# Performance work log

Hardware: AMD Instinct MI355X
Metric: run time of the kernel (lower is better)

Reference implementation:

```python
import jax, jax.numpy as jnp
from jax import lax
import numpy as np

B, T, H, K = 32, 512, 2048, 128


def setup_inputs() -> dict:
    key = jax.random.key(0)
    k1, k2, k3, k4, k5, k6, k7 = jax.random.split(key, 7)
    hiddens = jax.random.normal(k1, (B, T, H), dtype=jnp.float32)
    mask = jnp.ones((B, T), dtype=jnp.int32)  # mask[:,0] must be on (torchcrf)
    labels = jax.random.randint(k2, (B, T), 0, K)
    W = jax.random.normal(k3, (H, K), dtype=jnp.float32) * 0.02
    b = jnp.zeros((K,), dtype=jnp.float32)
    # torchcrf inits transitions uniform(-0.1, 0.1)
    start_transitions = jax.random.uniform(k4, (K,), minval=-0.1, maxval=0.1)
    end_transitions = jax.random.uniform(k5, (K,), minval=-0.1, maxval=0.1)
    transitions = jax.random.uniform(k6, (K, K), minval=-0.1, maxval=0.1)
    return {"hiddens": hiddens, "mask": mask, "labels": labels, "W": W, "b": b,
            "start_transitions": start_transitions, "end_transitions": end_transitions,
            "transitions": transitions}


def _crf_log_likelihood(emissions, tags, mask, start_t, end_t, trans):
    # emissions: [B,T,K], tags/mask: [B,T]
    Bn, Tn, Kn = emissions.shape
    maskf = mask.astype(emissions.dtype)
    # ---- numerator: score of the gold path ----
    score = start_t[tags[:, 0]] + emissions[jnp.arange(Bn), 0, tags[:, 0]]
    prev, cur = tags[:, :-1], tags[:, 1:]
    emit_cur = jnp.take_along_axis(emissions[:, 1:], cur[..., None], axis=-1)[..., 0]
    score = score + jnp.sum((trans[prev, cur] + emit_cur) * maskf[:, 1:], axis=1)
    last_idx = mask.sum(axis=1).astype(jnp.int32) - 1
    last_tags = jnp.take_along_axis(tags, last_idx[:, None], axis=1)[:, 0]
    score = score + end_t[last_tags]
    # ---- denominator: log partition via stable logsumexp scan ----
    def step(alpha, inp):
        emit_t, m_t = inp  # [B,K], [B]
        nxt = jax.nn.logsumexp(alpha[:, :, None] + trans[None] + emit_t[:, None, :], axis=1)
        alpha = jnp.where(m_t[:, None] > 0, nxt, alpha)
        return alpha, None
    alpha0 = start_t[None, :] + emissions[:, 0]
    emits = jnp.swapaxes(emissions[:, 1:], 0, 1)  # [T-1,B,K]
    ms = jnp.swapaxes(mask[:, 1:], 0, 1)          # [T-1,B]
    alpha, _ = lax.scan(step, alpha0, (emits, ms))
    logZ = jax.nn.logsumexp(alpha + end_t[None, :], axis=1)
    return score - logZ


def _viterbi_decode(emissions, mask, start_t, end_t, trans):
    Bn, Tn, Kn = emissions.shape
    tag_ids = jnp.arange(Kn, dtype=jnp.int32)
    def step(score, inp):
        emit_t, m_t = inp
        cand = score[:, :, None] + trans[None]          # [B,K,K] prev->cur
        bp = jnp.argmax(cand, axis=1).astype(jnp.int32)  # [B,K]
        best = jnp.max(cand, axis=1) + emit_t
        on = m_t[:, None] > 0
        new_score = jnp.where(on, best, score)
        bp = jnp.where(on, bp, tag_ids[None, :])  # identity for padded steps
        return new_score, bp
    score0 = start_t[None, :] + emissions[:, 0]
    emits = jnp.swapaxes(emissions[:, 1:], 0, 1)
    ms = jnp.swapaxes(mask[:, 1:], 0, 1)
    score, history = lax.scan(step, score0, (emits, ms))  # history: [T-1,B,K]
    last_tag = jnp.argmax(score + end_t[None, :], axis=1).astype(jnp.int32)  # [B]
    def back(tag, bp_t):
        tag = jnp.take_along_axis(bp_t, tag[:, None], axis=1)[:, 0]
        return tag, tag
    _, tags_prev = lax.scan(back, last_tag, history, reverse=True)  # [T-1,B]
    tags = jnp.concatenate([tags_prev, last_tag[None, :]], axis=0)  # [T,B]
    return jnp.swapaxes(tags, 0, 1)  # [B,T]


def reference(hiddens, mask, labels, W, b, start_transitions, end_transitions, transitions):
    logits = jnp.einsum('bth,hk->btk', hiddens, W) + b  # emission projection
    decode = _viterbi_decode(logits, mask, start_transitions, end_transitions, transitions)
    llh = _crf_log_likelihood(logits, labels, mask, start_transitions, end_transitions, transitions)
    loss = -jnp.mean(llh)  # -1 * crf(..., reduction='mean')
    return (decode, loss)
```

## Files before the change

kernel.cpp:

```cpp
#include <hip/hip_runtime.h>
#include <hip/hip_bf16.h>
#include <math.h>

#define BB 32
#define TT 512
#define HH 2048
#define KK 128
#define CH 8

__device__ __forceinline__ float quad_add(float x) {
    int a = __builtin_amdgcn_update_dpp(0, __float_as_int(x), 0xB1, 0xF, 0xF, true);
    x += __int_as_float(a);
    int b = __builtin_amdgcn_update_dpp(0, __float_as_int(x), 0x4E, 0xF, 0xF, true);
    x += __int_as_float(b);
    return x;
}
__device__ __forceinline__ float quad_max(float x) {
    int a = __builtin_amdgcn_update_dpp(0, __float_as_int(x), 0xB1, 0xF, 0xF, true);
    x = fmaxf(x, __int_as_float(a));
    int b = __builtin_amdgcn_update_dpp(0, __float_as_int(x), 0x4E, 0xF, 0xF, true);
    x = fmaxf(x, __int_as_float(b));
    return x;
}

__global__ __launch_bounds__(512) void gemm_k(const float* __restrict__ hid,
                                              const float* __restrict__ Wm,
                                              const float* __restrict__ bias,
                                              float* __restrict__ logits,
                                              float* __restrict__ loss_slot) {
    __shared__ union {
        struct { float As[4][16][72]; float Bs[4][16][132]; } s;
        float4 red[16][128];
    } sm;
    const int tid = threadIdx.x, bid = blockIdx.x;
    if (bid == 0 && tid == 0) loss_slot[0] = 0.0f;
    const int g = tid >> 7, lt = tid & 127;
    const int rowBase = bid * 64;
    const int rowg = lt >> 4, colg = lt & 15;
    const int arow = lt >> 1, ahq = lt & 1;

    float acc[8][8];
#pragma unroll
    for (int i = 0; i < 8; i++)
#pragma unroll
        for (int j = 0; j < 8; j++) acc[i][j] = 0.0f;

    const float* hA = hid + (size_t)(rowBase + arow) * HH + g * 512 + ahq * 8;

    float4 a0, a1, bv[4];
    {
        const int h0 = g * 512;
        a0 = *(const float4*)(hA);
        a1 = *(const float4*)(hA + 4);
#pragma unroll
        for (int r = 0; r < 4; ++r) {
            int idx = r * 128 + lt;
            bv[r] = *(const float4*)(Wm + (size_t)(h0 + (idx >> 5)) * KK + (idx & 31) * 4);
        }
    }

    for (int it = 0; it < 32; ++it) {
        __syncthreads();
        const int hb = ahq * 8;
        sm.s.As[g][hb + 0][arow] = a0.x;
        sm.s.As[g][hb + 1][arow] = a0.y;
        sm.s.As[g][hb + 2][arow] = a0.z;
        sm.s.As[g][hb + 3][arow] = a0.w;
        sm.s.As[g][hb + 4][arow] = a1.x;
        sm.s.As[g][hb + 5][arow] = a1.y;
        sm.s.As[g][hb + 6][arow] = a1.z;
        sm.s.As[g][hb + 7][arow] = a1.w;
#pragma unroll
        for (int r = 0; r < 4; ++r) {
            int idx = r * 128 + lt;
            *(float4*)&sm.s.Bs[g][idx >> 5][(idx & 31) * 4] = bv[r];
        }
        __syncthreads();
        if (it + 1 < 32) {
            const int h0 = g * 512 + (it + 1) * 16;
            a0 = *(const float4*)(hA + (it + 1) * 16);
            a1 = *(const float4*)(hA + (it + 1) * 16 + 4);
#pragma unroll
            for (int r = 0; r < 4; ++r) {
                int idx = r * 128 + lt;
                bv[r] = *(const float4*)(Wm + (size_t)(h0 + (idx >> 5)) * KK + (idx & 31) * 4);
            }
        }
#pragma unroll
        for (int h = 0; h < 16; ++h) {
            float4 aL = *(const float4*)&sm.s.As[g][h][rowg * 8];
            float4 aH = *(const float4*)&sm.s.As[g][h][rowg * 8 + 4];
            float4 b0 = *(const float4*)&sm.s.Bs[g][h][colg * 4];
            float4 b1 = *(const float4*)&sm.s.Bs[g][h][64 + colg * 4];
            float ar[8] = {aL.x, aL.y, aL.z, aL.w, aH.x, aH.y, aH.z, aH.w};
            float br[8] = {b0.x, b0.y, b0.z, b0.w, b1.x, b1.y, b1.z, b1.w};
#pragma unroll
            for (int i = 0; i < 8; i++)
#pragma unroll
                for (int j = 0; j < 8; j++) acc[i][j] = fmaf(ar[i], br[j], acc[i][j]);
        }
    }
    __syncthreads();
    for (int gp = 1; gp <= 3; ++gp) {
        if (g == gp) {
#pragma unroll
            for (int i = 0; i < 8; ++i) {
                sm.red[i * 2][lt] = make_float4(acc[i][0], acc[i][1], acc[i][2], acc[i][3]);
                sm.red[i * 2 + 1][lt] = make_float4(acc[i][4], acc[i][5], acc[i][6], acc[i][7]);
            }
        }
        __syncthreads();
        if (g == 0) {
#pragma unroll
            for (int i = 0; i < 8; ++i) {
                float4 r0 = sm.red[i * 2][lt];
                float4 r1 = sm.red[i * 2 + 1][lt];
                acc[i][0] += r0.x; acc[i][1] += r0.y; acc[i][2] += r0.z; acc[i][3] += r0.w;
                acc[i][4] += r1.x; acc[i][5] += r1.y; acc[i][6] += r1.z; acc[i][7] += r1.w;
            }
        }
        __syncthreads();
    }
    if (g == 0) {
        float4 bb0 = *(const float4*)(bias + colg * 4);
        float4 bb1 = *(const float4*)(bias + 64 + colg * 4);
#pragma unroll
        for (int i = 0; i < 8; ++i) {
            int row = rowBase + rowg * 8 + i;
            *(float4*)(logits + (size_t)row * KK + colg * 4) =
                make_float4(acc[i][0] + bb0.x, acc[i][1] + bb0.y, acc[i][2] + bb0.z, acc[i][3] + bb0.w);
            *(float4*)(logits + (size_t)row * KK + 64 + colg * 4) =
                make_float4(acc[i][4] + bb1.x, acc[i][5] + bb1.y, acc[i][6] + bb1.z, acc[i][7] + bb1.w);
        }
    }
}

struct SMemB {
    float ubuf[2][144];
    float red[4];
    float vbuf[128];
};

__global__ __launch_bounds__(256, 1) void scan_k(const float* __restrict__ logits,
                                                 const int* __restrict__ mask,
                                                 const int* __restrict__ labels,
                                                 const float* __restrict__ startT,
                                                 const float* __restrict__ endT,
                                                 const float* __restrict__ trans,
                                                 float* __restrict__ shist,
                                                 float* __restrict__ out) {
    __shared__ SMemB sm;
    const int tid = threadIdx.x;
    const int bid = blockIdx.x;
    const float L2E = 1.4426950408889634f;
    const int s = tid & 3;
    const int jb = tid >> 2;
    const int j0 = jb * 2;
    const int padw = j0 + 4 * (j0 >> 5);
    const int lane = tid & 63;
    const int NCHUNK = TT / CH;

    if (bid < BB) {
        const int b = bid;
        const float* lrow = logits + (size_t)b * TT * KK;
        unsigned long long mb[8];
#pragma unroll
        for (int c = 0; c < 8; ++c) mb[c] = __ballot(mask[b * TT + c * 64 + lane] != 0);
        float V0[32], V1[32];
#pragma unroll
        for (int k = 0; k < 32; k++) {
            V0[k] = exp2f(trans[(s * 32 + k) * KK + j0] * L2E);
            V1[k] = exp2f(trans[(s * 32 + k) * KK + j0 + 1] * L2E);
        }
        float a0_ = (startT[j0] + lrow[j0]) * L2E;
        float a1_ = (startT[j0 + 1] + lrow[j0 + 1]) * L2E;
        float OFF = (startT[0] + lrow[0]) * L2E;
        float S0_ = exp2f(a0_ - OFF);
        float S1_ = exp2f(a1_ - OFF);
        if (s == 0) {
            sm.ubuf[0][padw] = S0_;
            sm.ubuf[0][padw + 1] = S1_;
        }
        float2 emc[CH], emn[CH];
#pragma unroll
        for (int d = 0; d < CH; ++d) emc[d] = *(const float2*)(lrow + (size_t)d * KK + j0);
        __syncthreads();
        int cur = 0;
        for (int c = 0; c < NCHUNK; ++c) {
#pragma unroll
            for (int r = 0; r < CH; ++r) {
                const int t = c * CH + r;
                if (r == 0 && c + 1 < NCHUNK) {
#pragma unroll
                    for (int d = 0; d < CH; ++d)
                        emn[d] = *(const float2*)(lrow + (size_t)((c + 1) * CH + d) * KK + j0);
                }
                if (t > 0 && ((mb[t >> 6] >> (t & 63)) & 1ull)) {
                    const float* ub = &sm.ubuf[cur][s * 36];
                    float u00 = sm.ubuf[cur][0];
                    float uu[32];
#pragma unroll
                    for (int cc = 0; cc < 8; ++cc) {
                        float4 v = *(const float4*)(ub + cc * 4);
                        uu[cc * 4] = v.x; uu[cc * 4 + 1] = v.y; uu[cc * 4 + 2] = v.z; uu[cc * 4 + 3] = v.w;
                    }
                    float2 em = emc[r];
                    float p0e = 0.f, p0o = 0.f, p1e = 0.f, p1o = 0.f;
#pragma unroll
                    for (int k = 0; k < 32; k += 2) {
                        p0e = fmaf(uu[k], V0[k], p0e);
                        p1e = fmaf(uu[k], V1[k], p1e);
                        p0o = fmaf(uu[k + 1], V0[k + 1], p0o);
                        p1o = fmaf(uu[k + 1], V1[k + 1], p1o);
                    }
                    float w0 = quad_add(p0e + p0o);
                    float w1 = quad_add(p1e + p1o);
                    float rinv = __builtin_amdgcn_rcpf(u00);
                    OFF += log2f(u00);
                    S0_ = w0 * (exp2f(em.x * L2E) * rinv);
                    S1_ = w1 * (exp2f(em.y * L2E) * rinv);
                    if (s == 0) {
                        sm.ubuf[cur ^ 1][padw] = S0_;
                        sm.ubuf[cur ^ 1][padw + 1] = S1_;
                    }
                    cur ^= 1;
                }
                __syncthreads();
            }
#pragma unroll
            for (int d = 0; d < CH; ++d) emc[d] = emn[d];
        }
        if (s == 0) {
            sm.vbuf[j0] = log2f(S0_) + endT[j0] * L2E;
            sm.vbuf[j0 + 1] = log2f(S1_) + endT[j0 + 1] * L2E;
        }
        __syncthreads();

        float part = 0.0f;
        for (int tt = tid; tt < TT; tt += 256) {
            if (tt == 0) {
                int l0 = labels[b * TT];
                part += startT[l0] + lrow[l0];
            } else if (mask[b * TT + tt]) {
                int lc = labels[b * TT + tt];
                int lp = labels[b * TT + tt - 1];
                part += trans[lp * KK + lc] + lrow[(size_t)tt * KK + lc];
            }
        }
#pragma unroll
        for (int d = 1; d < 64; d <<= 1) part += __shfl_xor(part, d, 64);
        int wid = tid >> 6;
        if (lane == 0) sm.red[wid] = part;
        __syncthreads();
        if (tid < 64) {
            float v0 = sm.vbuf[tid], v1 = sm.vbuf[tid + 64];
            float mx = fmaxf(v0, v1);
#pragma unroll
            for (int d = 1; d < 64; d <<= 1) mx = fmaxf(mx, __shfl_xor(mx, d, 64));
            float p = exp2f(v0 - mx) + exp2f(v1 - mx);
#pragma unroll
            for (int d = 1; d < 64; d <<= 1) p += __shfl_xor(p, d, 64);
            if (tid == 0) {
                int total = 0;
#pragma unroll
                for (int c = 0; c < 8; ++c) total += __popcll(mb[c]);
                float score = sm.red[0] + sm.red[1] + sm.red[2] + sm.red[3];
                score += endT[labels[b * TT + total - 1]];
                float logZ = (OFF + mx + log2f(p)) * 0.6931471805599453f;
                float llh = score - logZ;
                atomicAdd(out + BB * TT, -llh * (1.0f / 32.0f));
            }
        }
    } else {
        const int b = bid - BB;
        const float* lrow = logits + (size_t)b * TT * KK;
        float* hist = shist + (size_t)b * TT * KK;
        unsigned long long mb[8];
#pragma unroll
        for (int c = 0; c < 8; ++c) mb[c] = __ballot(mask[b * TT + c * 64 + lane] != 0);
        float T0[32], T1[32];
#pragma unroll
        for (int k = 0; k < 32; k++) {
            T0[k] = trans[(s * 32 + k) * KK + j0];
            T1[k] = trans[(s * 32 + k) * KK + j0 + 1];
        }
        float s0_ = startT[j0] + lrow[j0];
        float s1_ = startT[j0 + 1] + lrow[j0 + 1];
        if (s == 0) {
            sm.ubuf[0][padw] = s0_;
            sm.ubuf[0][padw + 1] = s1_;
        } else if (s == 1) {
            *(float2*)(hist + j0) = make_float2(s0_, s1_);
        }
        float2 emc[CH], emn[CH], hb[CH];
#pragma unroll
        for (int d = 0; d < CH; ++d) emc[d] = *(const float2*)(lrow + (size_t)d * KK + j0);
        __syncthreads();
        int cur = 0;
        for (int c = 0; c < NCHUNK; ++c) {
#pragma unroll
            for (int r = 0; r < CH; ++r) {
                const int t = c * CH + r;
                if (r == 0 && c + 1 < NCHUNK) {
#pragma unroll
                    for (int d = 0; d < CH; ++d)
                        emn[d] = *(const float2*)(lrow + (size_t)((c + 1) * CH + d) * KK + j0);
                }
                if (t > 0 && ((mb[t >> 6] >> (t & 63)) & 1ull)) {
                    const float* ub = &sm.ubuf[cur][s * 36];
                    float uu[32];
#pragma unroll
                    for (int cc = 0; cc < 8; ++cc) {
                        float4 v = *(const float4*)(ub + cc * 4);
                        uu[cc * 4] = v.x; uu[cc * 4 + 1] = v.y; uu[cc * 4 + 2] = v.z; uu[cc * 4 + 3] = v.w;
                    }
                    float2 em = emc[r];
                    float m0a = -3.0e38f, m0b = -3.0e38f, m1a = -3.0e38f, m1b = -3.0e38f;
#pragma unroll
                    for (int k = 0; k < 32; k += 4) {
                        m0a = fmaxf(m0a, fmaxf(uu[k] + T0[k], uu[k + 1] + T0[k + 1]));
                        m0b = fmaxf(m0b, fmaxf(uu[k + 2] + T0[k + 2], uu[k + 3] + T0[k + 3]));
                        m1a = fmaxf(m1a, fmaxf(uu[k] + T1[k], uu[k + 1] + T1[k + 1]));
                        m1b = fmaxf(m1b, fmaxf(uu[k + 2] + T1[k + 2], uu[k + 3] + T1[k + 3]));
                    }
                    float m0 = quad_max(fmaxf(m0a, m0b));
                    float m1 = quad_max(fmaxf(m1a, m1b));
                    s0_ = m0 + em.x;
                    s1_ = m1 + em.y;
                    if (s == 0) {
                        sm.ubuf[cur ^ 1][padw] = s0_;
                        sm.ubuf[cur ^ 1][padw + 1] = s1_;
                    }
                    cur ^= 1;
                }
                hb[r] = make_float2(s0_, s1_);
                __syncthreads();
            }
            if (s == 1) {
#pragma unroll
                for (int r = 0; r < CH; ++r)
                    *(float2*)(hist + (size_t)(c * CH + r) * KK + j0) = hb[r];
            }
#pragma unroll
            for (int d = 0; d < CH; ++d) emc[d] = emn[d];
        }
    }
}

__global__ __launch_bounds__(256) void bp_k(const float* __restrict__ shist,
                                            const float* __restrict__ trans,
                                            const int* __restrict__ mask,
                                            unsigned char* __restrict__ bp) {
    const int t = blockIdx.x + 1;
    const int tid = threadIdx.x;
    const int j = tid & 127, bg = tid >> 7;
    __shared__ float sc[BB][KK];
#pragma unroll
    for (int r = 0; r < 4; ++r) {
        int f = tid + r * 256;
        int bb2 = f >> 5, c4 = (f & 31) * 4;
        *(float4*)&sc[bb2][c4] = *(const float4*)&shist[(size_t)bb2 * TT * KK + (size_t)(t - 1) * KK + c4];
    }
    __syncthreads();
    float m[16];
    int idx[16];
#pragma unroll
    for (int c = 0; c < 16; c++) { m[c] = -3.0e38f; idx[c] = 0; }
    for (int i4 = 0; i4 < 32; ++i4) {
        const int ib = i4 * 4;
        float tr0 = trans[(ib + 0) * KK + j];
        float tr1 = trans[(ib + 1) * KK + j];
        float tr2 = trans[(ib + 2) * KK + j];
        float tr3 = trans[(ib + 3) * KK + j];
#pragma unroll
        for (int c = 0; c < 16; c++) {
            float4 s4 = *(const float4*)&sc[bg + 2 * c][ib];
            float c0 = s4.x + tr0, c1 = s4.y + tr1, c2 = s4.z + tr2, c3 = s4.w + tr3;
            if (c0 > m[c]) { m[c] = c0; idx[c] = ib; }
            if (c1 > m[c]) { m[c] = c1; idx[c] = ib + 1; }
            if (c2 > m[c]) { m[c] = c2; idx[c] = ib + 2; }
            if (c3 > m[c]) { m[c] = c3; idx[c] = ib + 3; }
        }
    }
#pragma unroll
    for (int c = 0; c < 16; c++) {
        int bb2 = bg + 2 * c;
        int v = idx[c];
        if (mask[bb2 * TT + t] == 0) v = j;
        bp[(size_t)bb2 * TT * KK + (size_t)t * KK + j] = (unsigned char)v;
    }
}

__global__ __launch_bounds__(512) void bt_k(const float* __restrict__ shist,
                                            const float* __restrict__ endT,
                                            const unsigned char* __restrict__ bp,
                                            float* __restrict__ out) {
    const int b = blockIdx.x;
    const int tid = threadIdx.x;
    const int lane = tid & 63, w = tid >> 6;
    __shared__ float cb[128];
    __shared__ int tagbuf[512];
    __shared__ int handoff;
    if (tid < 128) cb[tid] = shist[(size_t)b * TT * KK + (size_t)(TT - 1) * KK + tid] + endT[tid];
    __syncthreads();
    if (tid == 0) {
        float mm = cb[0];
        int bi = 0;
        for (int i = 1; i < 128; i++)
            if (cb[i] > mm) { mm = cb[i]; bi = i; }
        tagbuf[TT - 1] = bi;
        handoff = bi;
    }
    unsigned int reg[64];
    const unsigned char* bpb = bp + (size_t)b * TT * KK;
#pragma unroll
    for (int r = 0; r < 64; r++) {
        int t_row = w * 64 + 1 + r;
        unsigned int v = 0;
        if (t_row < TT) v = *(const unsigned short*)(bpb + (size_t)t_row * KK + lane * 2);
        reg[r] = v;
    }
    __syncthreads();
    for (int ph = 7; ph >= 0; --ph) {
        if (w == ph) {
            int tag = handoff;
#pragma unroll
            for (int r = 63; r >= 0; --r) {
                int t_row = ph * 64 + 1 + r;
                if (t_row < TT) {
                    unsigned int vv = (unsigned int)__shfl((int)reg[r], tag >> 1, 64);
                    tag = (int)((vv >> ((tag & 1) * 8)) & 0xffu);
                    if (lane == 0) tagbuf[t_row - 1] = tag;
                }
            }
            if (lane == 0) handoff = tag;
        }
        __syncthreads();
    }
    out[b * TT + tid] = (float)tagbuf[tid];
}

extern "C" void kernel_launch(void* const* d_in, const int* in_sizes, int n_in,
                              void* d_out, int out_size, void* d_ws, size_t ws_size,
                              hipStream_t stream) {
    const float* hid = (const float*)d_in[0];
    const int* mask = (const int*)d_in[1];
    const int* labels = (const int*)d_in[2];
    const float* Wm = (const float*)d_in[3];
    const float* bias = (const float*)d_in[4];
    const float* startT = (const float*)d_in[5];
    const float* endT = (const float*)d_in[6];
    const float* trans = (const float*)d_in[7];
    float* out = (float*)d_out;
    char* ws = (char*)d_ws;

    float* logits = (float*)ws;
    float* shist = (float*)(ws + 8388608);
    unsigned char* bp = (unsigned char*)(ws + 16777216);

    gemm_k<<<256, 512, 0, stream>>>(hid, Wm, bias, logits, out + BB * TT);
    scan_k<<<64, 256, 0, stream>>>(logits, mask, labels, startT, endT, trans, shist, out);
    bp_k<<<TT - 1, 256, 0, stream>>>(shist, trans, mask, bp);
    bt_k<<<BB, 512, 0, stream>>>(shist, endT, bp, out);
}
```

Baseline: 623.1 us.

## Split CRF forward scan into forward/backward halves meeting at midpoint

The log-partition scan is split into a forward-alpha pass over the first 256 steps and a backward-beta pass over the last 256 steps, each run by its own block. Their scaled state vectors and offsets are stored in the output buffer and combined in the backtrace kernel, which computes logZ and the loss. This roughly halves the serial chain length of the partition scan, so it no longer exceeds the Viterbi scan. Barriers are replaced with a custom s_barrier that waits only on LDS counters. The cost is more blocks and reliance on the output buffer as scratch space before the tags overwrite it. The backward-half mask handling also differs subtly from the reference for padded sequences.

```diff
diff --git a/kernel.cpp b/kernel.cpp
--- a/kernel.cpp
+++ b/kernel.cpp
@@ -7,6 +7,12 @@
 #define HH 2048
 #define KK 128
 #define CH 8
+#define NC 32
+#define NCV 64
+
+#define WS_LOGITS 0
+#define WS_SHIST  8388608u
+#define WS_BP     16777216u
 
 __device__ __forceinline__ float quad_add(float x) {
     int a = __builtin_amdgcn_update_dpp(0, __float_as_int(x), 0xB1, 0xF, 0xF, true);
@@ -21,6 +27,14 @@
     int b = __builtin_amdgcn_update_dpp(0, __float_as_int(x), 0x4E, 0xF, 0xF, true);
     x = fmaxf(x, __int_as_float(b));
     return x;
+}
+
+__device__ __forceinline__ void step_barrier() {
+    __builtin_amdgcn_sched_barrier(0);
+    asm volatile("s_waitcnt lgkmcnt(0)" ::: "memory");
+    __builtin_amdgcn_sched_barrier(0);
+    __builtin_amdgcn_s_barrier();
+    __builtin_amdgcn_sched_barrier(0);
 }
 
 __global__ __launch_bounds__(512) void gemm_k(const float* __restrict__ hid,
@@ -138,7 +152,6 @@
 struct SMemB {
     float ubuf[2][144];
     float red[4];
-    float vbuf[128];
 };
 
 __global__ __launch_bounds__(256, 1) void scan_k(const float* __restrict__ logits,
@@ -158,7 +171,6 @@
     const int j0 = jb * 2;
     const int padw = j0 + 4 * (j0 >> 5);
     const int lane = tid & 63;
-    const int NCHUNK = TT / CH;
 
     if (bid < BB) {
         const int b = bid;
@@ -186,11 +198,11 @@
         for (int d = 0; d < CH; ++d) emc[d] = *(const float2*)(lrow + (size_t)d * KK + j0);
         __syncthreads();
         int cur = 0;
-        for (int c = 0; c < NCHUNK; ++c) {
+        for (int c = 0; c < NC; ++c) {
 #pragma unroll
             for (int r = 0; r < CH; ++r) {
                 const int t = c * CH + r;
-                if (r == 0 && c + 1 < NCHUNK) {
+                if (r == 0 && c + 1 < NC) {
 #pragma unroll
                     for (int d = 0; d < CH; ++d)
                         emn[d] = *(const float2*)(lrow + (size_t)((c + 1) * CH + d) * KK + j0);
@@ -225,16 +237,16 @@
                     }
                     cur ^= 1;
                 }
-                __syncthreads();
+                step_barrier();
             }
 #pragma unroll
             for (int d = 0; d < CH; ++d) emc[d] = emn[d];
         }
         if (s == 0) {
-            sm.vbuf[j0] = log2f(S0_) + endT[j0] * L2E;
-            sm.vbuf[j0 + 1] = log2f(S1_) + endT[j0 + 1] * L2E;
-        }
-        __syncthreads();
+            out[b * TT + j0] = S0_;
+            out[b * TT + j0 + 1] = S1_;
+        }
+        if (tid == 0) out[b * TT + 384] = OFF;
 
         float part = 0.0f;
         for (int tt = tid; tt < TT; tt += 256) {
@@ -252,27 +264,92 @@
         int wid = tid >> 6;
         if (lane == 0) sm.red[wid] = part;
         __syncthreads();
-        if (tid < 64) {
-            float v0 = sm.vbuf[tid], v1 = sm.vbuf[tid + 64];
-            float mx = fmaxf(v0, v1);
-#pragma unroll
-            for (int d = 1; d < 64; d <<= 1) mx = fmaxf(mx, __shfl_xor(mx, d, 64));
-            float p = exp2f(v0 - mx) + exp2f(v1 - mx);
-#pragma unroll
-            for (int d = 1; d < 64; d <<= 1) p += __shfl_xor(p, d, 64);
-            if (tid == 0) {
-                int total = 0;
-#pragma unroll
-                for (int c = 0; c < 8; ++c) total += __popcll(mb[c]);
-                float score = sm.red[0] + sm.red[1] + sm.red[2] + sm.red[3];
-                score += endT[labels[b * TT + total - 1]];
-                float logZ = (OFF + mx + log2f(p)) * 0.6931471805599453f;
-                float llh = score - logZ;
-                atomicAdd(out + BB * TT, -llh * (1.0f / 32.0f));
-            }
-        }
+        if (tid == 0) {
+            int total = 0;
+#pragma unroll
+            for (int c = 0; c < 8; ++c) total += __popcll(mb[c]);
+            float score = sm.red[0] + sm.red[1] + sm.red[2] + sm.red[3];
+            score += endT[labels[b * TT + total - 1]];
+            out[b * TT + 386] = score;
+        }
+    } else if (bid < 2 * BB) {
+        const int b = bid - BB;
+        const float* lrow = logits + (size_t)b * TT * KK;
+        unsigned long long mb[4];
+#pragma unroll
+        for (int c = 0; c < 4; ++c) mb[c] = __ballot(mask[b * TT + 256 + c * 64 + lane] != 0);
+        float V0[32], V1[32];
+#pragma unroll
+        for (int k = 0; k < 32; k++) {
+            V0[k] = exp2f(trans[j0 * KK + s * 32 + k] * L2E);
+            V1[k] = exp2f(trans[(j0 + 1) * KK + s * 32 + k] * L2E);
+        }
+        float OFF = endT[0] * L2E;
+        float S0_ = exp2f(endT[j0] * L2E - OFF);
+        float S1_ = exp2f(endT[j0 + 1] * L2E - OFF);
+        {
+            float2 e511 = *(const float2*)(lrow + (size_t)511 * KK + j0);
+            if (s == 0) {
+                sm.ubuf[0][padw] = exp2f(e511.x * L2E) * S0_;
+                sm.ubuf[0][padw + 1] = exp2f(e511.y * L2E) * S1_;
+            }
+        }
+        float2 emc[CH], emn[CH];
+#pragma unroll
+        for (int d = 0; d < CH; ++d) emc[d] = *(const float2*)(lrow + (size_t)(510 - d) * KK + j0);
+        __syncthreads();
+        int cur = 0;
+        for (int c = 0; c < NC; ++c) {
+#pragma unroll
+            for (int r = 0; r < CH; ++r) {
+                const int t = 511 - (c * CH + r);
+                if (r == 0 && c + 1 < NC) {
+#pragma unroll
+                    for (int d = 0; d < CH; ++d)
+                        emn[d] = *(const float2*)(lrow + (size_t)(510 - (c + 1) * CH - d) * KK + j0);
+                }
+                if ((mb[(t - 256) >> 6] >> ((t - 256) & 63)) & 1ull) {
+                    const float* ub = &sm.ubuf[cur][s * 36];
+                    float u00 = sm.ubuf[cur][0];
+                    float uu[32];
+#pragma unroll
+                    for (int cc = 0; cc < 8; ++cc) {
+                        float4 v = *(const float4*)(ub + cc * 4);
+                        uu[cc * 4] = v.x; uu[cc * 4 + 1] = v.y; uu[cc * 4 + 2] = v.z; uu[cc * 4 + 3] = v.w;
+                    }
+                    float p0e = 0.f, p0o = 0.f, p1e = 0.f, p1o = 0.f;
+#pragma unroll
+                    for (int k = 0; k < 32; k += 2) {
+                        p0e = fmaf(uu[k], V0[k], p0e);
+                        p1e = fmaf(uu[k], V1[k], p1e);
+                        p0o = fmaf(uu[k + 1], V0[k + 1], p0o);
+                        p1o = fmaf(uu[k + 1], V1[k + 1], p1o);
+                    }
+                    float w0 = quad_add(p0e + p0o);
+                    float w1 = quad_add(p1e + p1o);
+                    float rinv = __builtin_amdgcn_rcpf(u00);
+                    OFF += log2f(u00);
+                    S0_ = w0 * rinv;
+                    S1_ = w1 * rinv;
+                }
+                float2 em = emc[r];
+                if (s == 0) {
+                    sm.ubuf[cur ^ 1][padw] = exp2f(em.x * L2E) * S0_;
+                    sm.ubuf[cur ^ 1][padw + 1] = exp2f(em.y * L2E) * S1_;
+                }
+                cur ^= 1;
+                step_barrier();
+            }
+#pragma unroll
+            for (int d = 0; d < CH; ++d) emc[d] = emn[d];
+        }
+        if (s == 0) {
+            out[b * TT + 128 + j0] = S0_;
+            out[b * TT + 128 + j0 + 1] = S1_;
+        }
+        if (tid == 0) out[b * TT + 385] = OFF;
     } else {
-        const int b = bid - BB;
+        const int b = bid - 2 * BB;
         const float* lrow = logits + (size_t)b * TT * KK;
         float* hist = shist + (size_t)b * TT * KK;
         unsigned long long mb[8];
@@ -297,11 +374,11 @@
         for (int d = 0; d < CH; ++d) emc[d] = *(const float2*)(lrow + (size_t)d * KK + j0);
         __syncthreads();
         int cur = 0;
-        for (int c = 0; c < NCHUNK; ++c) {
+        for (int c = 0; c < NCV; ++c) {
 #pragma unroll
             for (int r = 0; r < CH; ++r) {
                 const int t = c * CH + r;
-                if (r == 0 && c + 1 < NCHUNK) {
+                if (r == 0 && c + 1 < NCV) {
 #pragma unroll
                     for (int d = 0; d < CH; ++d)
                         emn[d] = *(const float2*)(lrow + (size_t)((c + 1) * CH + d) * KK + j0);
@@ -334,7 +411,7 @@
                     cur ^= 1;
                 }
                 hb[r] = make_float2(s0_, s1_);
-                __syncthreads();
+                step_barrier();
             }
             if (s == 1) {
 #pragma unroll
@@ -399,9 +476,25 @@
     const int tid = threadIdx.x;
     const int lane = tid & 63, w = tid >> 6;
     __shared__ float cb[128];
+    __shared__ float pb[128];
     __shared__ int tagbuf[512];
     __shared__ int handoff;
-    if (tid < 128) cb[tid] = shist[(size_t)b * TT * KK + (size_t)(TT - 1) * KK + tid] + endT[tid];
+    if (tid < 128) {
+        cb[tid] = shist[(size_t)b * TT * KK + (size_t)(TT - 1) * KK + tid] + endT[tid];
+        pb[tid] = out[b * TT + tid] * out[b * TT + 128 + tid];
+    }
+    float offA = out[b * TT + 384];
+    float offB = out[b * TT + 385];
+    float score = out[b * TT + 386];
+    unsigned int reg[64];
+    const unsigned char* bpb = bp + (size_t)b * TT * KK;
+#pragma unroll
+    for (int r = 0; r < 64; r++) {
+        int t_row = w * 64 + 1 + r;
+        unsigned int v = 0;
+        if (t_row < TT) v = *(const unsigned short*)(bpb + (size_t)t_row * KK + lane * 2);
+        reg[r] = v;
+    }
     __syncthreads();
     if (tid == 0) {
         float mm = cb[0];
@@ -410,15 +503,11 @@
             if (cb[i] > mm) { mm = cb[i]; bi = i; }
         tagbuf[TT - 1] = bi;
         handoff = bi;
-    }
-    unsigned int reg[64];
-    const unsigned char* bpb = bp + (size_t)b * TT * KK;
-#pragma unroll
-    for (int r = 0; r < 64; r++) {
-        int t_row = w * 64 + 1 + r;
-        unsigned int v = 0;
-        if (t_row < TT) v = *(const unsigned short*)(bpb + (size_t)t_row * KK + lane * 2);
-        reg[r] = v;
+        float sum = 0.0f;
+        for (int i = 0; i < 128; i++) sum += pb[i];
+        float logZ = (offA + offB + log2f(sum)) * 0.6931471805599453f;
+        float llh = score - logZ;
+        atomicAdd(out + BB * TT, -llh * (1.0f / 32.0f));
     }
     __syncthreads();
     for (int ph = 7; ph >= 0; --ph) {
@@ -454,12 +543,12 @@
     float* out = (float*)d_out;
     char* ws = (char*)d_ws;
 
-    float* logits = (float*)ws;
-    float* shist = (float*)(ws + 8388608);
-    unsigned char* bp = (unsigned char*)(ws + 16777216);
+    float* logits = (float*)(ws + WS_LOGITS);
+    float* shist = (float*)(ws + WS_SHIST);
+    unsigned char* bp = (unsigned char*)(ws + WS_BP);
 
     gemm_k<<<256, 512, 0, stream>>>(hid, Wm, bias, logits, out + BB * TT);
-    scan_k<<<64, 256, 0, stream>>>(logits, mask, labels, startT, endT, trans, shist, out);
+    scan_k<<<96, 256, 0, stream>>>(logits, mask, labels, startT, endT, trans, shist, out);
     bp_k<<<TT - 1, 256, 0, stream>>>(shist, trans, mask, bp);
     bt_k<<<BB, 512, 0, stream>>>(shist, endT, bp, out);
 }
```

Result: no change. 623.6 us (+0.1%).
